# Kernel optimization log

Measured on AMD Instinct MI355X. Metric: run time of the kernel, lower is better.

The kernel has to match this reference:

```python
import jax, jax.numpy as jnp
import numpy as np

C_DIM = 512
N_TOKEN = 256
N_HEADS = 8
TOKEN_DIM = C_DIM // N_HEADS  # 64


def setup_inputs() -> dict:
    key = jax.random.key(0)
    ks = jax.random.split(key, 8)
    s = 1.0 / np.sqrt(C_DIM)
    W0 = jax.random.normal(ks[0], (4, 8192, C_DIM), dtype=jnp.float32)
    # learnable query tokens (xavier-uniform-ish)
    lim = np.sqrt(6.0 / (N_TOKEN + TOKEN_DIM))
    Q = jax.random.uniform(ks[1], (N_HEADS, N_TOKEN, TOKEN_DIM), minval=-lim, maxval=lim, dtype=jnp.float32)
    kv1_w = jax.random.normal(ks[2], (C_DIM, C_DIM), dtype=jnp.float32) * s
    kv1_b = jnp.zeros((C_DIM,), dtype=jnp.float32)
    qkv2_w = jax.random.normal(ks[3], (TOKEN_DIM, 2 * TOKEN_DIM), dtype=jnp.float32) * (1.0 / np.sqrt(TOKEN_DIM))
    q3_w = jax.random.normal(ks[4], (C_DIM, C_DIM), dtype=jnp.float32) * s
    q3_b = jnp.zeros((C_DIM,), dtype=jnp.float32)
    proj_w = jax.random.normal(ks[5], (C_DIM, C_DIM), dtype=jnp.float32) * s
    proj_b = jnp.zeros((C_DIM,), dtype=jnp.float32)
    return {"W0": W0, "Q": Q, "kv1_w": kv1_w, "kv1_b": kv1_b, "qkv2_w": qkv2_w,
            "q3_w": q3_w, "q3_b": q3_b, "proj_w": proj_w, "proj_b": proj_b}


def reference(W0, Q, kv1_w, kv1_b, qkv2_w, q3_w, q3_b, proj_w, proj_b):
    b, n, c = W0.shape
    h, td = N_HEADS, TOKEN_DIM
    scale = 1.0 / np.sqrt(td)
    # stage 1: compress n nodes into n_token tokens per head
    kv1 = (W0 @ kv1_w + kv1_b).reshape(b, n, h, td).transpose(0, 2, 1, 3)  # b h n c
    pw = jnp.einsum('hmc,bhnc->bhmn', Q, kv1) * scale
    pw = jax.nn.softmax(pw, axis=-1)
    proj_token = jnp.einsum('bhmn,bhnc->bhmc', pw, kv1)  # b h m c
    # stage 2: re-project tokens back to nodes
    kv2 = proj_token @ qkv2_w  # b h m 2c
    k, v = kv2[..., :td], kv2[..., td:]
    q3 = (W0 @ q3_w + q3_b).reshape(b, n, h, td).transpose(0, 2, 1, 3)  # b h n c
    rw = jax.nn.softmax(jnp.einsum('bhnc,bhmc->bhnm', q3, k) * scale, axis=-1)
    W = jnp.einsum('bhnm,bhmc->bhnc', rw, v)
    W = W.transpose(0, 2, 1, 3).reshape(b, n, c)  # b n (h c)
    return W @ proj_w + proj_b
```

## Files before the change

kernel.cpp:

```cpp
#include <hip/hip_runtime.h>
#include <hip/hip_bf16.h>


#define NB 4
#define NSEQ 8192
#define CD 512
#define NH 8
#define TD 64
#define NTOK 256
#define NSPLIT 16
#define NKEYS (NSEQ / NSPLIT)
#define LOG2E 1.44269504f

typedef unsigned short u16;
typedef unsigned int u32;
typedef __bf16 bf16x8 __attribute__((ext_vector_type(8)));
typedef float f32x4 __attribute__((ext_vector_type(4)));
typedef float f32x16 __attribute__((ext_vector_type(16)));

__device__ __forceinline__ u16 f2bf(float f){
  __hip_bfloat16 h = __float2bfloat16(f);
  u16 u; __builtin_memcpy(&u, &h, 2); return u;
}
__device__ __forceinline__ bf16x8 ld8(const u16* p){
  bf16x8 r; __builtin_memcpy(&r, p, 16); return r;
}
__device__ __forceinline__ f32x4 mfma16(bf16x8 a, bf16x8 b, f32x4 c){
  return __builtin_amdgcn_mfma_f32_16x16x32_bf16(a, b, c, 0, 0, 0);
}
__device__ __forceinline__ f32x16 mfma32(bf16x8 a, bf16x8 b, f32x16 c){
  return __builtin_amdgcn_mfma_f32_32x32x16_bf16(a, b, c, 0, 0, 0);
}
__device__ __forceinline__ float fexp2(float x){
  return __builtin_amdgcn_exp2f(x);
}
__device__ __forceinline__ void gload16(const u16* g, u16* l){
  __builtin_amdgcn_global_load_lds((const __attribute__((address_space(1))) void*)g,
                                   (__attribute__((address_space(3))) void*)l, 16, 0, 0);
}

__global__ void k_cvt_prep(const float* __restrict__ W0, u16* __restrict__ W0b,
                           const float* __restrict__ kv1_w, const float* __restrict__ q3_w,
                           const float* __restrict__ proj_w, const float* __restrict__ Q,
                           u16* __restrict__ kv1_wt, u16* __restrict__ q3_wt,
                           u16* __restrict__ proj_wt, u16* __restrict__ Qb){
  size_t i = (size_t)blockIdx.x * 256 + threadIdx.x;
  float4 v = ((const float4*)W0)[i];
  u16 w[4] = { f2bf(v.x), f2bf(v.y), f2bf(v.z), f2bf(v.w) };
  __builtin_memcpy(W0b + i*4, w, 8);
  if (i < (size_t)CD*CD){
    int k = (int)i >> 9, n = (int)i & 511;
    kv1_wt [n*CD + k] = f2bf(kv1_w[i]);
    q3_wt  [n*CD + k] = f2bf(q3_w[i] * (0.125f * LOG2E));
    proj_wt[n*CD + k] = f2bf(proj_w[i]);
    if (i < NH*NTOK*TD) Qb[i] = f2bf(Q[i] * (0.125f * LOG2E));
  }
}

__global__ __launch_bounds__(256, 2)
void k_gemm_dual(const u16* __restrict__ A, const u16* __restrict__ B1t,
                 const u16* __restrict__ B2t, const float* __restrict__ bias1,
                 const float* __restrict__ bias2, float bscale2,
                 u16* __restrict__ out1, u16* __restrict__ out2){
  __shared__ __attribute__((aligned(16))) u16 smem[3 * 128 * 64];
  u16* As  = smem;
  u16* B1s = smem + 128*64;
  u16* B2s = smem + 2*128*64;
  const int tid = threadIdx.x;
  const int lane = tid & 63, wave = tid >> 6;
  const int l15 = lane & 15, lg = lane >> 4;
  const int wm = (wave >> 1) * 64, wn = (wave & 1) * 64;
  const int bm = blockIdx.x, bn = blockIdx.y;
  const int lr = lane >> 3;
  const int csw = ((lane & 7) ^ lr) * 8;
  f32x4 acc1[4][4] = {}, acc2[4][4] = {};

#pragma unroll 1
  for (int k0 = 0; k0 < CD; k0 += 64){
    __syncthreads();
#pragma unroll
    for (int i = 0; i < 4; i++){
      int seg = i*4 + wave;
      int ch  = seg*8 + lr;
      gload16(A   + (size_t)(bm*128 + ch)*CD + k0 + csw, As  + seg*512);
      gload16(B1t + (size_t)(bn*128 + ch)*CD + k0 + csw, B1s + seg*512);
      gload16(B2t + (size_t)(bn*128 + ch)*CD + k0 + csw, B2s + seg*512);
    }
    __syncthreads();
#pragma unroll
    for (int ks = 0; ks < 2; ks++){
      bf16x8 af[4], b1f[4], b2f[4];
#pragma unroll
      for (int mf = 0; mf < 4; mf++){
        int R = wm + mf*16 + l15;
        int off = R*64 + (((ks*4 + lg) ^ (R & 7)) << 3);
        af[mf] = ld8(As + off);
      }
#pragma unroll
      for (int nf = 0; nf < 4; nf++){
        int R = wn + nf*16 + l15;
        int off = R*64 + (((ks*4 + lg) ^ (R & 7)) << 3);
        b1f[nf] = ld8(B1s + off);
        b2f[nf] = ld8(B2s + off);
      }
#pragma unroll
      for (int mf = 0; mf < 4; mf++)
#pragma unroll
        for (int nf = 0; nf < 4; nf++){
          acc1[mf][nf] = mfma16(af[mf], b1f[nf], acc1[mf][nf]);
          acc2[mf][nf] = mfma16(af[mf], b2f[nf], acc2[mf][nf]);
        }
    }
  }

  u16 (*cs)[136] = (u16 (*)[136])smem;
  const int erow = tid >> 1, ecol0 = (tid & 1) * 64;
  __syncthreads();
#pragma unroll
  for (int nf = 0; nf < 4; nf++){
    int col = wn + nf*16 + l15;
    float bv = bias1[bn*128 + col];
#pragma unroll
    for (int mf = 0; mf < 4; mf++){
      int row = wm + mf*16 + lg*4;
#pragma unroll
      for (int q = 0; q < 4; q++) cs[row + q][col] = f2bf(acc1[mf][nf][q] + bv);
    }
  }
  __syncthreads();
#pragma unroll
  for (int e = 0; e < 8; e++){
    int4 v; __builtin_memcpy(&v, &cs[erow][ecol0 + e*8], 16);
    __builtin_memcpy(out1 + (size_t)(bm*128 + erow)*CD + bn*128 + ecol0 + e*8, &v, 16);
  }
  __syncthreads();
#pragma unroll
  for (int nf = 0; nf < 4; nf++){
    int col = wn + nf*16 + l15;
    float bv = bias2[bn*128 + col] * bscale2;
#pragma unroll
    for (int mf = 0; mf < 4; mf++){
      int row = wm + mf*16 + lg*4;
#pragma unroll
      for (int q = 0; q < 4; q++) cs[row + q][col] = f2bf(acc2[mf][nf][q] + bv);
    }
  }
  __syncthreads();
#pragma unroll
  for (int e = 0; e < 8; e++){
    int4 v; __builtin_memcpy(&v, &cs[erow][ecol0 + e*8], 16);
    __builtin_memcpy(out2 + (size_t)(bm*128 + erow)*CD + bn*128 + ecol0 + e*8, &v, 16);
  }
}

__global__ __launch_bounds__(256, 2)
void k_gemm_proj(const u16* __restrict__ A, const u16* __restrict__ Bt,
                 const float* __restrict__ bias, float* __restrict__ outp){
  __shared__ __attribute__((aligned(16))) u16 smem[2 * 128 * 64];
  u16* As = smem;
  u16* Bs = smem + 128*64;
  const int tid = threadIdx.x;
  const int lane = tid & 63, wave = tid >> 6;
  const int l15 = lane & 15, lg = lane >> 4;
  const int wm = (wave >> 1) * 64, wn = (wave & 1) * 64;
  const int bm = blockIdx.x, bn = blockIdx.y;
  const int lr = lane >> 3;
  const int csw = ((lane & 7) ^ lr) * 8;
  f32x4 acc[4][4] = {};

#pragma unroll 1
  for (int k0 = 0; k0 < CD; k0 += 64){
    __syncthreads();
#pragma unroll
    for (int i = 0; i < 4; i++){
      int seg = i*4 + wave;
      int ch  = seg*8 + lr;
      gload16(A  + (size_t)(bm*128 + ch)*CD + k0 + csw, As + seg*512);
      gload16(Bt + (size_t)(bn*128 + ch)*CD + k0 + csw, Bs + seg*512);
    }
    __syncthreads();
#pragma unroll
    for (int ks = 0; ks < 2; ks++){
      bf16x8 af[4], bfr[4];
#pragma unroll
      for (int mf = 0; mf < 4; mf++){
        int R = wm + mf*16 + l15;
        int off = R*64 + (((ks*4 + lg) ^ (R & 7)) << 3);
        af[mf] = ld8(As + off);
      }
#pragma unroll
      for (int nf = 0; nf < 4; nf++){
        int R = wn + nf*16 + l15;
        int off = R*64 + (((ks*4 + lg) ^ (R & 7)) << 3);
        bfr[nf] = ld8(Bs + off);
      }
#pragma unroll
      for (int mf = 0; mf < 4; mf++)
#pragma unroll
        for (int nf = 0; nf < 4; nf++)
          acc[mf][nf] = mfma16(af[mf], bfr[nf], acc[mf][nf]);
    }
  }
#pragma unroll
  for (int nf = 0; nf < 4; nf++){
    int col = bn*128 + wn + nf*16 + l15;
    float bv = bias[col];
#pragma unroll
    for (int mf = 0; mf < 4; mf++){
      int row = bm*128 + wm + mf*16 + lg*4;
#pragma unroll
      for (int q = 0; q < 4; q++)
        outp[(size_t)(row + q)*CD + col] = acc[mf][nf][q] + bv;
    }
  }
}

__global__ __launch_bounds__(256, 4)
void k_attn1(const u16* __restrict__ kv1, const u16* __restrict__ Qb,
             float* __restrict__ o_part, float* __restrict__ ml_part){
  __shared__ __attribute__((aligned(16))) u16 kvs[64][72];
  __shared__ __attribute__((aligned(16))) u16 kvts[64][72];
  const int tid = threadIdx.x, lane = tid & 63, wave = tid >> 6;
  const int bh = blockIdx.x, mt = blockIdx.y, s = blockIdx.z;
  const int b = bh >> 3, h = bh & 7;
  const int l31 = lane & 31, hi = lane >> 5;
  const int m0 = mt*128 + wave*32;

  bf16x8 bq[4];
#pragma unroll
  for (int ks = 0; ks < 4; ks++)
    bq[ks] = ld8(Qb + (size_t)(h*NTOK + m0 + l31)*TD + ks*16 + hi*8);

  float mrun = -1e30f, srun = 0.f;
  f32x16 o0 = {}, o1 = {};

#pragma unroll 1
  for (int c = 0; c < NKEYS/64; c++){
    const int nc = s*NKEYS + c*64;
    __syncthreads();
    {
      int r = tid >> 2, sg = tid & 3, seg = sg * 16;
      const u16* src = kv1 + (size_t)(b*NSEQ + nc + r)*CD + h*TD + seg;
      int4 v0 = *(const int4*)src;
      int4 v1 = *(const int4*)(src + 8);
      __builtin_memcpy(&kvs[r][seg],     &v0, 16);
      __builtin_memcpy(&kvs[r][seg + 8], &v1, 16);
      u32 tr[8];
      __builtin_memcpy(tr,     &v0, 16);
      __builtin_memcpy(tr + 4, &v1, 16);
      u32 t1[8], t2[8];
#pragma unroll
      for (int i = 0; i < 8; i++) t1[i] = (sg & 1) ? tr[(i + 1) & 7] : tr[i];
#pragma unroll
      for (int i = 0; i < 8; i++) t2[i] = (sg & 2) ? t1[(i + 2) & 7] : t1[i];
#pragma unroll
      for (int j2 = 0; j2 < 8; j2++){
        int jj = (2*j2 + 2*sg) & 15;
        kvts[seg + jj][r]     = (u16)(t2[j2] & 0xffff);
        kvts[seg + jj + 1][r] = (u16)(t2[j2] >> 16);
      }
    }
    __syncthreads();
#pragma unroll
    for (int sub = 0; sub < 2; sub++){
      f32x16 t = {};
      __builtin_amdgcn_s_setprio(1);
#pragma unroll
      for (int ks = 0; ks < 4; ks++){
        bf16x8 ak = ld8(&kvs[sub*32 + l31][ks*16 + hi*8]);
        t = mfma32(ak, bq[ks], t);
      }
      __builtin_amdgcn_s_setprio(0);
      float c0 = fmaxf(fmaxf(t[0], t[1]),  fmaxf(t[2], t[3]));
      float c1 = fmaxf(fmaxf(t[4], t[5]),  fmaxf(t[6], t[7]));
      float c2 = fmaxf(fmaxf(t[8], t[9]),  fmaxf(t[10], t[11]));
      float c3 = fmaxf(fmaxf(t[12], t[13]), fmaxf(t[14], t[15]));
      float cm = fmaxf(fmaxf(c0, c1), fmaxf(c2, c3));
      cm = fmaxf(cm, __shfl_xor(cm, 32, 64));
      if (!__all(cm <= mrun + 11.5416f)){
        float mnew = fmaxf(mrun, cm);
        float corr = fexp2(mrun - mnew);
        srun *= corr;
#pragma unroll
        for (int r = 0; r < 16; r++){ o0[r] *= corr; o1[r] *= corr; }
        mrun = mnew;
      }
      u32 w[8], x[8];
      float ls = 0.f;
#pragma unroll
      for (int j = 0; j < 8; j++){
        float e0 = fexp2(t[2*j]     - mrun);
        float e1 = fexp2(t[2*j + 1] - mrun);
        ls += e0 + e1;
        w[j] = (u32)f2bf(e0) | ((u32)f2bf(e1) << 16);
      }
      srun += ls;
#pragma unroll
      for (int j = 0; j < 8; j++) x[j] = __shfl_xor(w[j], 32, 64);
      __builtin_amdgcn_s_setprio(1);
#pragma unroll
      for (int c2i = 0; c2i < 2; c2i++){
        u32 arr[4];
        arr[0] = hi ? x[4*c2i + 2] : w[4*c2i + 0];
        arr[1] = hi ? x[4*c2i + 3] : w[4*c2i + 1];
        arr[2] = hi ? w[4*c2i + 2] : x[4*c2i + 0];
        arr[3] = hi ? w[4*c2i + 3] : x[4*c2i + 1];
        bf16x8 pb; __builtin_memcpy(&pb, arr, 16);
        bf16x8 av0 = ld8(&kvts[l31][sub*32 + c2i*16 + hi*8]);
        bf16x8 av1 = ld8(&kvts[l31 + 32][sub*32 + c2i*16 + hi*8]);
        o0 = mfma32(av0, pb, o0);
        o1 = mfma32(av1, pb, o1);
      }
      __builtin_amdgcn_s_setprio(0);
    }
  }
  float rs = srun + __shfl_xor(srun, 32, 64);

  const size_t pbase = (size_t)(bh*NSPLIT + s);
  float* qrow = o_part + (pbase*NTOK + m0 + l31)*TD;
#pragma unroll
  for (int g = 0; g < 4; g++){
    float4 v0 = make_float4(o0[4*g+0], o0[4*g+1], o0[4*g+2], o0[4*g+3]);
    *(float4*)(qrow + 8*g + 4*hi) = v0;
    float4 v1 = make_float4(o1[4*g+0], o1[4*g+1], o1[4*g+2], o1[4*g+3]);
    *(float4*)(qrow + 32 + 8*g + 4*hi) = v1;
  }
  if (hi == 0){
    ml_part[(pbase*2)*NTOK + m0 + l31]     = mrun;
    ml_part[(pbase*2 + 1)*NTOK + m0 + l31] = rs;
  }
}

__global__ __launch_bounds__(256, 2)
void k_comb(const float* __restrict__ o_part, const float* __restrict__ ml_part,
            const float* __restrict__ qkv2_w, u16* __restrict__ kb, u16* __restrict__ vtb){
  __shared__ float w2[TD*2*TD];
  __shared__ float osh[16][68];
  const int tid = threadIdx.x;
  const int bh = blockIdx.x >> 4, mtile = blockIdx.x & 15;
  const int m0 = mtile * 16;
  for (int i = tid; i < TD*2*TD/4; i += 256) ((float4*)w2)[i] = ((const float4*)qkv2_w)[i];

  const int mi = tid >> 4, tj = tid & 15;
  const int m = m0 + mi;
  float M = -1e30f;
#pragma unroll
  for (int s = 0; s < NSPLIT; s++)
    M = fmaxf(M, ml_part[(size_t)((bh*NSPLIT + s)*2)*NTOK + m]);
  float4 acc = make_float4(0.f,0.f,0.f,0.f);
  float denom = 0.f;
#pragma unroll 1
  for (int s = 0; s < NSPLIT; s++){
    size_t base = (size_t)(bh*NSPLIT + s);
    float w = fexp2(ml_part[(base*2)*NTOK + m] - M);
    denom += ml_part[(base*2 + 1)*NTOK + m] * w;
    float4 v = ((const float4*)(o_part + (base*NTOK + m)*TD))[tj];
    acc.x += w*v.x; acc.y += w*v.y; acc.z += w*v.z; acc.w += w*v.w;
  }
  float inv = 1.f / denom;
  osh[mi][tj*4+0] = acc.x*inv; osh[mi][tj*4+1] = acc.y*inv;
  osh[mi][tj*4+2] = acc.z*inv; osh[mi][tj*4+3] = acc.w*inv;
  __syncthreads();
  const int j0 = tj * 8;
  float o8[8] = {};
#pragma unroll
  for (int t = 0; t < TD; t++){
    float ov = osh[mi][t];
#pragma unroll
    for (int jj = 0; jj < 8; jj++) o8[jj] += ov * w2[t*2*TD + j0 + jj];
  }
  if (j0 < TD){
#pragma unroll
    for (int jj = 0; jj < 8; jj++)
      kb[(size_t)(bh*NTOK + m)*TD + j0 + jj] = f2bf(o8[jj]);
  } else {
#pragma unroll
    for (int jj = 0; jj < 8; jj++)
      vtb[(size_t)(bh*TD + (j0 - TD + jj))*NTOK + m] = f2bf(o8[jj]);
  }
}

__global__ __launch_bounds__(256, 2)
void k_attn2(const u16* __restrict__ q3, const u16* __restrict__ kb,
             const u16* __restrict__ vtb, u16* __restrict__ Wout){
  __shared__ __attribute__((aligned(16))) u16 buf[32768];
  u16* kbs = buf;
  u16* vts = buf + 16384;
  const int tid = threadIdx.x, lane = tid & 63, wave = tid >> 6;
  const int bh = blockIdx.x >> 6, nt = blockIdx.x & 63;
  const int b = bh >> 3, h = bh & 7;
  const int l31 = lane & 31, hi = lane >> 5;
  const int n0 = nt * 128 + wave * 32;

  bf16x8 bq[4];
#pragma unroll
  for (int ks = 0; ks < 4; ks++)
    bq[ks] = ld8(q3 + (size_t)(b*NSEQ + n0 + l31)*CD + h*TD + ks*16 + hi*8);

  {
    const u16* ksrc = kb + (size_t)bh*NTOK*TD;
#pragma unroll
    for (int it = 0; it < 8; it++){
      int idx = it*256 + tid;
      int r = idx >> 3, g = idx & 7;
      int4 v; __builtin_memcpy(&v, ksrc + r*64 + g*8, 16);
      __builtin_memcpy(kbs + r*64 + ((g ^ (r & 7)) << 3), &v, 16);
    }
    const u16* vsrc = vtb + (size_t)bh*TD*NTOK;
#pragma unroll
    for (int it = 0; it < 8; it++){
      int idx = it*256 + tid;
      int t = idx >> 5, g = idx & 31;
      int4 v; __builtin_memcpy(&v, vsrc + t*256 + g*8, 16);
      __builtin_memcpy(vts + t*256 + ((g ^ (t & 31)) << 3), &v, 16);
    }
  }
  __syncthreads();

  f32x16 p[8] = {};
  __builtin_amdgcn_s_setprio(1);
#pragma unroll
  for (int kt = 0; kt < 8; kt++){
#pragma unroll
    for (int ks = 0; ks < 4; ks++){
      int r = kt*32 + l31, g = ks*2 + hi;
      bf16x8 ak = ld8(kbs + r*64 + ((g ^ (r & 7)) << 3));
      p[kt] = mfma32(ak, bq[ks], p[kt]);
    }
  }
  __builtin_amdgcn_s_setprio(0);

  float mx0 = -1e30f, mx1 = -1e30f, mx2 = -1e30f, mx3 = -1e30f;
#pragma unroll
  for (int kt = 0; kt < 8; kt++){
#pragma unroll
    for (int r = 0; r < 16; r += 4){
      mx0 = fmaxf(mx0, p[kt][r+0]); mx1 = fmaxf(mx1, p[kt][r+1]);
      mx2 = fmaxf(mx2, p[kt][r+2]); mx3 = fmaxf(mx3, p[kt][r+3]);
    }
  }
  float m = fmaxf(fmaxf(mx0, mx1), fmaxf(mx2, mx3));
  m = fmaxf(m, __shfl_xor(m, 32, 64));
  float s0 = 0.f, s1 = 0.f, s2 = 0.f, s3 = 0.f;
#pragma unroll
  for (int kt = 0; kt < 8; kt++){
#pragma unroll
    for (int r = 0; r < 16; r += 4){
      float e0 = fexp2(p[kt][r+0] - m); p[kt][r+0] = e0; s0 += e0;
      float e1 = fexp2(p[kt][r+1] - m); p[kt][r+1] = e1; s1 += e1;
      float e2 = fexp2(p[kt][r+2] - m); p[kt][r+2] = e2; s2 += e2;
      float e3 = fexp2(p[kt][r+3] - m); p[kt][r+3] = e3; s3 += e3;
    }
  }
  float rs = (s0 + s1) + (s2 + s3);
  rs += __shfl_xor(rs, 32, 64);
  const float inv = 1.f / rs;

  f32x16 o0 = {}, o1 = {};
#pragma unroll
  for (int kt = 0; kt < 8; kt++){
    u32 w[8], x[8];
#pragma unroll
    for (int j = 0; j < 8; j++){
      u32 lo = f2bf(p[kt][2*j]);
      u32 hh = f2bf(p[kt][2*j + 1]);
      w[j] = lo | (hh << 16);
    }
#pragma unroll
    for (int j = 0; j < 8; j++) x[j] = __shfl_xor(w[j], 32, 64);
    __builtin_amdgcn_s_setprio(1);
#pragma unroll
    for (int c = 0; c < 2; c++){
      u32 arr[4];
      arr[0] = hi ? x[4*c + 2] : w[4*c + 0];
      arr[1] = hi ? x[4*c + 3] : w[4*c + 1];
      arr[2] = hi ? w[4*c + 2] : x[4*c + 0];
      arr[3] = hi ? w[4*c + 3] : x[4*c + 1];
      bf16x8 pb; __builtin_memcpy(&pb, arr, 16);
      int g = kt*4 + c*2 + hi;
      bf16x8 av0 = ld8(vts + l31*256        + ((g ^ l31) << 3));
      bf16x8 av1 = ld8(vts + (l31+32)*256   + ((g ^ l31) << 3));
      o0 = mfma32(av0, pb, o0);
      o1 = mfma32(av1, pb, o1);
    }
    __builtin_amdgcn_s_setprio(0);
  }

  __syncthreads();
  u16 (*osh)[32][68] = (u16 (*)[32][68])buf;
#pragma unroll
  for (int r = 0; r < 16; r++){
    int row = (r & 3) + 8*(r >> 2) + 4*hi;
    osh[wave][l31][row]      = f2bf(o0[r] * inv);
    osh[wave][l31][32 + row] = f2bf(o1[r] * inv);
  }
  const u16* src = &osh[wave][l31][hi*32];
  int4 v0, v1, v2, v3;
  __builtin_memcpy(&v0, src,      16);
  __builtin_memcpy(&v1, src + 8,  16);
  __builtin_memcpy(&v2, src + 16, 16);
  __builtin_memcpy(&v3, src + 24, 16);
  u16* dst = Wout + (size_t)(b*NSEQ + n0 + l31)*CD + h*TD + hi*32;
  __builtin_memcpy(dst,      &v0, 16);
  __builtin_memcpy(dst + 8,  &v1, 16);
  __builtin_memcpy(dst + 16, &v2, 16);
  __builtin_memcpy(dst + 24, &v3, 16);
}

extern "C" void kernel_launch(void* const* d_in, const int* in_sizes, int n_in,
                              void* d_out, int out_size, void* d_ws, size_t ws_size,
                              hipStream_t stream){
  const float* W0     = (const float*)d_in[0];
  const float* Q      = (const float*)d_in[1];
  const float* kv1_w  = (const float*)d_in[2];
  const float* kv1_b  = (const float*)d_in[3];
  const float* qkv2_w = (const float*)d_in[4];
  const float* q3_w   = (const float*)d_in[5];
  const float* q3_b   = (const float*)d_in[6];
  const float* proj_w = (const float*)d_in[7];
  const float* proj_b = (const float*)d_in[8];
  (void)in_sizes; (void)n_in; (void)out_size; (void)ws_size;

  char* ws = (char*)d_ws;
  u16*   W0b     = (u16*)  (ws);
  u16*   kv1_ws  = (u16*)  (ws + ((size_t)32<<20));
  float* o_part  = (float*)(ws + ((size_t)64<<20));
  float* ml_part = (float*)(ws + ((size_t)96<<20));
  u16*   kv1_wt  = (u16*)  (ws + ((size_t)97<<20));
  u16*   q3_wt   = (u16*)  (ws + ((size_t)97<<20) + (1<<19));
  u16*   proj_wt = (u16*)  (ws + ((size_t)98<<20));
  u16*   Qb      = (u16*)  (ws + ((size_t)98<<20) + (1<<19));
  u16*   kb      = (u16*)  (ws + ((size_t)99<<20));
  u16*   vtb     = (u16*)  (ws + ((size_t)100<<20));
  u16*   W_ws    = (u16*)  (ws + ((size_t)32<<20));
  u16*   q3s     = (u16*)  d_out;

  k_cvt_prep<<<16384, 256, 0, stream>>>(W0, W0b, kv1_w, q3_w, proj_w, Q,
                                        kv1_wt, q3_wt, proj_wt, Qb);
  k_gemm_dual<<<dim3(256,4), 256, 0, stream>>>(W0b, kv1_wt, q3_wt, kv1_b, q3_b,
                                               0.125f * LOG2E, kv1_ws, q3s);
  k_attn1<<<dim3(NB*NH, 2, NSPLIT), 256, 0, stream>>>(kv1_ws, Qb, o_part, ml_part);
  k_comb<<<NB*NH*16, 256, 0, stream>>>(o_part, ml_part, qkv2_w, kb, vtb);
  k_attn2<<<NB*NH*64, 256, 0, stream>>>(q3s, kb, vtb, W_ws);
  k_gemm_proj<<<dim3(256,4), 256, 0, stream>>>(W_ws, proj_wt, proj_b, (float*)d_out);
}
```

Baseline: 200.0 us.

## Double-buffer dual GEMM loads and halve N tile to 64 columns

Restructures the dual kv1/q3 projection GEMM so the next K-slice's global-to-LDS loads are issued into a second buffer while the current slice is computed, synchronised with vmcnt waits and raw barriers. The per-block N tile shrinks from 128 to 64 columns, doubling the grid and halving the accumulator registers per wave. The epilogue now writes bf16 results straight from registers instead of staging through LDS for coalesced stores. The aim is to hide load latency and raise occupancy. The cost is that the A tile is re-read by twice as many blocks, and the direct stores are scattered 2-byte writes.

```diff
diff --git a/kernel.cpp b/kernel.cpp
--- a/kernel.cpp
+++ b/kernel.cpp
@@ -62,94 +62,89 @@
                  const u16* __restrict__ B2t, const float* __restrict__ bias1,
                  const float* __restrict__ bias2, float bscale2,
                  u16* __restrict__ out1, u16* __restrict__ out2){
-  __shared__ __attribute__((aligned(16))) u16 smem[3 * 128 * 64];
-  u16* As  = smem;
-  u16* B1s = smem + 128*64;
-  u16* B2s = smem + 2*128*64;
+  __shared__ __attribute__((aligned(16))) u16 buf[2 * 16384];
   const int tid = threadIdx.x;
   const int lane = tid & 63, wave = tid >> 6;
   const int l15 = lane & 15, lg = lane >> 4;
-  const int wm = (wave >> 1) * 64, wn = (wave & 1) * 64;
+  const int wm = (wave >> 1) * 64, wn = (wave & 1) * 32;
   const int bm = blockIdx.x, bn = blockIdx.y;
   const int lr = lane >> 3;
   const int csw = ((lane & 7) ^ lr) * 8;
-  f32x4 acc1[4][4] = {}, acc2[4][4] = {};
-
+  f32x4 acc1[4][2] = {}, acc2[4][2] = {};
+
+#define STAGE_DUAL(bi, kk) do {                                               \
+    u16* Ab_  = buf + (bi)*16384;                                             \
+    u16* B1b_ = Ab_ + 8192;                                                   \
+    u16* B2b_ = B1b_ + 4096;                                                  \
+    _Pragma("unroll")                                                         \
+    for (int i_ = 0; i_ < 4; i_++){                                           \
+      int seg_ = i_*4 + wave;                                                 \
+      int ch_  = seg_*8 + lr;                                                 \
+      gload16(A + (size_t)(bm*128 + ch_)*CD + (kk) + csw, Ab_ + seg_*512);    \
+    }                                                                         \
+    _Pragma("unroll")                                                         \
+    for (int i_ = 0; i_ < 2; i_++){                                           \
+      int seg_ = i_*4 + wave;                                                 \
+      int ch_  = seg_*8 + lr;                                                 \
+      gload16(B1t + (size_t)(bn*64 + ch_)*CD + (kk) + csw, B1b_ + seg_*512);  \
+      gload16(B2t + (size_t)(bn*64 + ch_)*CD + (kk) + csw, B2b_ + seg_*512);  \
+    }                                                                         \
+  } while(0)
+
+  STAGE_DUAL(0, 0);
 #pragma unroll 1
-  for (int k0 = 0; k0 < CD; k0 += 64){
-    __syncthreads();
-#pragma unroll
-    for (int i = 0; i < 4; i++){
-      int seg = i*4 + wave;
-      int ch  = seg*8 + lr;
-      gload16(A   + (size_t)(bm*128 + ch)*CD + k0 + csw, As  + seg*512);
-      gload16(B1t + (size_t)(bn*128 + ch)*CD + k0 + csw, B1s + seg*512);
-      gload16(B2t + (size_t)(bn*128 + ch)*CD + k0 + csw, B2s + seg*512);
-    }
-    __syncthreads();
+  for (int t = 0; t < 8; t++){
+    const int cur = t & 1;
+    if (t < 7) STAGE_DUAL(cur ^ 1, (t + 1) * 64);
+    if (t < 7) asm volatile("s_waitcnt vmcnt(8)" ::: "memory");
+    else       asm volatile("s_waitcnt vmcnt(0)" ::: "memory");
+    __builtin_amdgcn_sched_barrier(0);
+    __builtin_amdgcn_s_barrier();
+    u16* Ab  = buf + cur*16384;
+    u16* B1b = Ab + 8192;
+    u16* B2b = B1b + 4096;
 #pragma unroll
     for (int ks = 0; ks < 2; ks++){
-      bf16x8 af[4], b1f[4], b2f[4];
+      bf16x8 af[4], b1f[2], b2f[2];
 #pragma unroll
       for (int mf = 0; mf < 4; mf++){
         int R = wm + mf*16 + l15;
         int off = R*64 + (((ks*4 + lg) ^ (R & 7)) << 3);
-        af[mf] = ld8(As + off);
-      }
-#pragma unroll
-      for (int nf = 0; nf < 4; nf++){
+        af[mf] = ld8(Ab + off);
+      }
+#pragma unroll
+      for (int nf = 0; nf < 2; nf++){
         int R = wn + nf*16 + l15;
         int off = R*64 + (((ks*4 + lg) ^ (R & 7)) << 3);
-        b1f[nf] = ld8(B1s + off);
-        b2f[nf] = ld8(B2s + off);
+        b1f[nf] = ld8(B1b + off);
+        b2f[nf] = ld8(B2b + off);
       }
 #pragma unroll
       for (int mf = 0; mf < 4; mf++)
 #pragma unroll
-        for (int nf = 0; nf < 4; nf++){
+        for (int nf = 0; nf < 2; nf++){
           acc1[mf][nf] = mfma16(af[mf], b1f[nf], acc1[mf][nf]);
           acc2[mf][nf] = mfma16(af[mf], b2f[nf], acc2[mf][nf]);
         }
     }
-  }
-
-  u16 (*cs)[136] = (u16 (*)[136])smem;
-  const int erow = tid >> 1, ecol0 = (tid & 1) * 64;
-  __syncthreads();
-#pragma unroll
-  for (int nf = 0; nf < 4; nf++){
-    int col = wn + nf*16 + l15;
-    float bv = bias1[bn*128 + col];
+    __builtin_amdgcn_s_barrier();
+  }
+#undef STAGE_DUAL
+
+#pragma unroll
+  for (int nf = 0; nf < 2; nf++){
+    int col = bn*64 + wn + nf*16 + l15;
+    float bv1 = bias1[col];
+    float bv2 = bias2[col] * bscale2;
 #pragma unroll
     for (int mf = 0; mf < 4; mf++){
-      int row = wm + mf*16 + lg*4;
-#pragma unroll
-      for (int q = 0; q < 4; q++) cs[row + q][col] = f2bf(acc1[mf][nf][q] + bv);
-    }
-  }
-  __syncthreads();
-#pragma unroll
-  for (int e = 0; e < 8; e++){
-    int4 v; __builtin_memcpy(&v, &cs[erow][ecol0 + e*8], 16);
-    __builtin_memcpy(out1 + (size_t)(bm*128 + erow)*CD + bn*128 + ecol0 + e*8, &v, 16);
-  }
-  __syncthreads();
-#pragma unroll
-  for (int nf = 0; nf < 4; nf++){
-    int col = wn + nf*16 + l15;
-    float bv = bias2[bn*128 + col] * bscale2;
-#pragma unroll
-    for (int mf = 0; mf < 4; mf++){
-      int row = wm + mf*16 + lg*4;
-#pragma unroll
-      for (int q = 0; q < 4; q++) cs[row + q][col] = f2bf(acc2[mf][nf][q] + bv);
-    }
-  }
-  __syncthreads();
-#pragma unroll
-  for (int e = 0; e < 8; e++){
-    int4 v; __builtin_memcpy(&v, &cs[erow][ecol0 + e*8], 16);
-    __builtin_memcpy(out2 + (size_t)(bm*128 + erow)*CD + bn*128 + ecol0 + e*8, &v, 16);
+      int row = bm*128 + wm + mf*16 + lg*4;
+#pragma unroll
+      for (int q = 0; q < 4; q++){
+        out1[(size_t)(row + q)*CD + col] = f2bf(acc1[mf][nf][q] + bv1);
+        out2[(size_t)(row + q)*CD + col] = f2bf(acc2[mf][nf][q] + bv2);
+      }
+    }
   }
 }
 
@@ -537,8 +532,8 @@
 
   k_cvt_prep<<<16384, 256, 0, stream>>>(W0, W0b, kv1_w, q3_w, proj_w, Q,
                                         kv1_wt, q3_wt, proj_wt, Qb);
-  k_gemm_dual<<<dim3(256,4), 256, 0, stream>>>(W0b, kv1_wt, q3_wt, kv1_b, q3_b,
-                                               0.125f * LOG2E, kv1_ws, q3s);
+  k_gemm_dual<<<dim3(256, 8), 256, 0, stream>>>(W0b, kv1_wt, q3_wt, kv1_b, q3_b,
+                                                0.125f * LOG2E, kv1_ws, q3s);
   k_attn1<<<dim3(NB*NH, 2, NSPLIT), 256, 0, stream>>>(kv1_ws, Qb, o_part, ml_part);
   k_comb<<<NB*NH*16, 256, 0, stream>>>(o_part, ml_part, qkv2_w, kb, vtb);
   k_attn2<<<NB*NH*64, 256, 0, stream>>>(q3s, kb, vtb, W_ws);
```

After: 199.3 us. About the same (-0.4%).
